# Performance work log

Hardware: AMD Instinct MI355X
Metric: run time of the kernel (lower is better)

Reference implementation:

```python
import jax, jax.numpy as jnp
import numpy as np
from jax import lax

B, S, E, H, V, C = 1024, 512, 128, 256, 128, 18


def setup_inputs() -> dict:
    key = jax.random.key(0)
    ks = jax.random.split(key, 12)
    x_in = jax.random.randint(ks[0], (B, S), 0, V, dtype=jnp.int32)
    x_lengths = jax.random.randint(ks[1], (B,), 1, S + 1, dtype=jnp.int32)
    emb = jax.random.normal(ks[2], (V, E), dtype=jnp.float32)
    emb = emb.at[0].set(0.0)  # padding_idx=0 row is zero
    k = 1.0 / np.sqrt(H)
    W_ih = jax.random.uniform(ks[3], (H, E), jnp.float32, -k, k)
    W_hh = jax.random.uniform(ks[4], (H, H), jnp.float32, -k, k)
    b_ih = jax.random.uniform(ks[5], (H,), jnp.float32, -k, k)
    b_hh = jax.random.uniform(ks[6], (H,), jnp.float32, -k, k)
    fc1_w = jax.random.uniform(ks[7], (H, H), jnp.float32, -k, k)
    fc1_b = jax.random.uniform(ks[8], (H,), jnp.float32, -k, k)
    kc = 1.0 / np.sqrt(H)
    fc2_w = jax.random.uniform(ks[9], (C, H), jnp.float32, -kc, kc)
    fc2_b = jax.random.uniform(ks[10], (C,), jnp.float32, -kc, kc)
    return dict(x_in=x_in, x_lengths=x_lengths, emb=emb, W_ih=W_ih, W_hh=W_hh,
                b_ih=b_ih, b_hh=b_hh, fc1_w=fc1_w, fc1_b=fc1_b,
                fc2_w=fc2_w, fc2_b=fc2_b)


def reference(x_in, x_lengths, emb, W_ih, W_hh, b_ih, b_hh, fc1_w, fc1_b, fc2_w, fc2_b):
    # Embedding lookup: [B,S] -> [B,S,E]
    x_emb = emb[x_in]
    # time-major for scan: [S,B,E]
    xt = jnp.transpose(x_emb, (1, 0, 2))

    def step(h, x_t):
        # Elman RNNCell: h' = tanh(x W_ih^T + b_ih + h W_hh^T + b_hh)
        h_new = jnp.tanh(x_t @ W_ih.T + b_ih + h @ W_hh.T + b_hh)
        return h_new, h_new

    h0 = jnp.zeros((x_in.shape[0], W_hh.shape[0]), dtype=x_emb.dtype)
    _, hiddens = lax.scan(step, h0, xt)  # [S,B,H]

    # column_gather: last valid hidden state per example
    idx = x_lengths.astype(jnp.int32) - 1
    y = hiddens[idx, jnp.arange(x_in.shape[0])]  # [B,H]

    # dropout omitted (deterministic / eval-mode reference)
    y = jax.nn.relu(y @ fc1_w.T + fc1_b)
    y = y @ fc2_w.T + fc2_b  # [B,C]; apply_activator=False
    return y
```

## Files before the change

kernel.cpp:

```cpp
#include <hip/hip_runtime.h>

#define Bb 1024
#define Ss 512
#define Ee 128
#define Hh 256
#define Vv 128
#define Cc 18

#define HB1  2048
#define YOFF 4096
#define ZOFF 8192

typedef __attribute__((ext_vector_type(8))) short short8;
typedef __attribute__((ext_vector_type(4))) float f32x4;
typedef __attribute__((ext_vector_type(2))) int int2v;

__device__ __forceinline__ unsigned short f2bf(float f) {
  union { float f; unsigned u; } v; v.f = f;
  return (unsigned short)((v.u + 0x7FFFu + ((v.u >> 16) & 1u)) >> 16);
}

__device__ __forceinline__ f32x4 mfma16(short8 a, short8 b, f32x4 c) {
  return __builtin_amdgcn_mfma_f32_16x16x32_bf16(a, b, c, 0, 0, 0);
}

__device__ __forceinline__ float ftanh(float x) {
  float e2 = __expf(2.0f * x);
  return 1.0f - 2.0f * __builtin_amdgcn_rcpf(e2 + 1.0f);
}

__device__ __forceinline__ unsigned cvtpk(float a, float b) {
  unsigned r;
  asm("v_cvt_pk_bf16_f32 %0, %1, %2" : "=v"(r) : "v"(a), "v"(b));
  return r;
}

__device__ __forceinline__ void load_wfrags2(const float* __restrict__ W, int j0, int l15, int g,
                                             short8 wfrag[2][8]) {
#pragma unroll
  for (int mt = 0; mt < 2; ++mt) {
    const float* wrow = W + (j0 + mt * 16 + l15) * Hh;
#pragma unroll
    for (int kt = 0; kt < 8; ++kt) {
      const float* wp = wrow + kt * 32 + g * 8;
      f32x4 a = *(const f32x4*)(wp);
      f32x4 b = *(const f32x4*)(wp + 4);
      short8 f;
      f[0] = (short)f2bf(a.x); f[1] = (short)f2bf(a.y);
      f[2] = (short)f2bf(a.z); f[3] = (short)f2bf(a.w);
      f[4] = (short)f2bf(b.x); f[5] = (short)f2bf(b.y);
      f[6] = (short)f2bf(b.z); f[7] = (short)f2bf(b.w);
      wfrag[mt][kt] = f;
    }
  }
}

__global__ void prep_T(const float* __restrict__ emb, const float* __restrict__ W_ih,
                       const float* __restrict__ b_ih, const float* __restrict__ b_hh,
                       float* __restrict__ T) {
  __shared__ float elds[Ee];
  const int v = blockIdx.x, j = threadIdx.x;
  if (j < Ee) elds[j] = emb[v * Ee + j];
  __syncthreads();
  float s = b_ih[j] + b_hh[j];
  const float* wr = W_ih + j * Ee;
#pragma unroll 8
  for (int e = 0; e < Ee; e += 4) {
    f32x4 w = *(const f32x4*)(wr + e);
    f32x4 x = *(const f32x4*)(elds + e);
    s += w.x * x.x + w.y * x.y + w.z * x.z + w.w * x.w;
  }
  T[v * Hh + j] = s;
}

template <int PAR>
__device__ __forceinline__ void step_phase(char* smem, const short8 (&wf)[2][8],
                                           const int (&roff)[8], const int (&woff)[2],
                                           const float* __restrict__ T,
                                           const int* __restrict__ xrow,
                                           int t, int mylen, int j0, int g, bool vr,
                                           f32x4 (&tcur)[2], int& xv_use, int& xv_inf) {
  char* RB = smem + (PAR ? HB1 : 0);
  char* WB = smem + (PAR ? 0 : HB1);

  const float* tp = T + xv_use * Hh + j0 + g * 4;
  f32x4 tn0 = *(const f32x4*)(tp);
  f32x4 tn1 = *(const f32x4*)(tp + 16);
  const int xv_new = xrow[min(t + 3, Ss - 1)];

  short8 hf[8];
  hf[0] = *(const short8*)(RB + roff[0]);
  hf[1] = *(const short8*)(RB + roff[1]);

  f32x4 aA[2], aB[2];
  const f32x4 Z4 = {0.f, 0.f, 0.f, 0.f};
  aA[0] = tcur[0]; aA[1] = tcur[1]; aB[0] = Z4; aB[1] = Z4;

#pragma unroll
  for (int kt = 0; kt < 8; ++kt) {
    if (kt < 6) hf[kt + 2] = *(const short8*)(RB + roff[kt + 2]);
    if ((kt & 1) == 0) {
      aA[0] = mfma16(wf[0][kt], hf[kt], aA[0]);
      aA[1] = mfma16(wf[1][kt], hf[kt], aA[1]);
    } else {
      aB[0] = mfma16(wf[0][kt], hf[kt], aB[0]);
      aB[1] = mfma16(wf[1][kt], hf[kt], aB[1]);
    }
  }

  const bool emit = (t == mylen - 1);
#pragma unroll
  for (int mt = 0; mt < 2; ++mt) {
    float s0 = aA[mt].x + aB[mt].x;
    float s1 = aA[mt].y + aB[mt].y;
    float s2 = aA[mt].z + aB[mt].z;
    float s3 = aA[mt].w + aB[mt].w;
    int2v pk;
    pk.x = (int)cvtpk(ftanh(s0), ftanh(s1));
    pk.y = (int)cvtpk(ftanh(s2), ftanh(s3));
    if (vr) {
      *(int2v*)(WB + woff[mt]) = pk;
      if (emit) *(int2v*)(smem + YOFF + woff[mt]) = pk;
    }
  }

  tcur[0] = tn0; tcur[1] = tn1;
  xv_use = xv_inf;
  xv_inf = xv_new;

  asm volatile("s_waitcnt lgkmcnt(0)" ::: "memory");
  __builtin_amdgcn_sched_barrier(0);
  __builtin_amdgcn_s_barrier();
  __builtin_amdgcn_sched_barrier(0);
}

__global__ __launch_bounds__(512, 2)
void rnn_fused(const int* __restrict__ x_in, const int* __restrict__ x_len,
               const float* __restrict__ W_hh, const float* __restrict__ T,
               const float* __restrict__ fc1_w, const float* __restrict__ fc1_b,
               const float* __restrict__ fc2_w, const float* __restrict__ fc2_b,
               float* __restrict__ out) {
  __shared__ __align__(16) char smem[12288];

  const int tid  = threadIdx.x;
  const int lane = tid & 63;
  const int wave = tid >> 6;
  const int l15  = lane & 15;
  const int g    = lane >> 4;
  const int j0   = wave * 32;
  const int grow = blockIdx.x * 4;
  const int r    = l15;
  const int rr   = r & 3;
  const bool vr  = (r < 4);

  short8 wfrag[2][8];
  load_wfrags2(W_hh, j0, l15, g, wfrag);

  const int mylen = x_len[grow + rr];
  int maxlen = 1;
#pragma unroll
  for (int i = 0; i < 4; ++i) maxlen = max(maxlen, x_len[grow + i]);

  ((int*)smem)[tid < 512 ? tid : 0] = 0;

  int roff[8], woff[2];
#pragma unroll
  for (int kt = 0; kt < 8; ++kt) roff[kt] = rr * 512 + ((kt * 64 + g * 16) ^ (rr << 6));
#pragma unroll
  for (int mt = 0; mt < 2; ++mt)
    woff[mt] = rr * 512 + (((j0 + mt * 16 + g * 4) * 2) ^ (rr << 6));

  const int* xrow = x_in + (grow + rr) * Ss;
  f32x4 tcur[2];
  {
    const int xv0 = xrow[0];
    const float* tp = T + xv0 * Hh + j0 + g * 4;
    tcur[0] = *(const f32x4*)(tp);
    tcur[1] = *(const f32x4*)(tp + 16);
  }
  int xv_use = xrow[min(1, Ss - 1)];
  int xv_inf = xrow[min(2, Ss - 1)];

  __syncthreads();

  const int mx2 = (maxlen + 1) & ~1;
  for (int t = 0; t < mx2; t += 2) {
    step_phase<0>(smem, wfrag, roff, woff, T, xrow, t,     mylen, j0, g, vr, tcur, xv_use, xv_inf);
    step_phase<1>(smem, wfrag, roff, woff, T, xrow, t + 1, mylen, j0, g, vr, tcur, xv_use, xv_inf);
  }

  short8 ffrag[2][8];
  load_wfrags2(fc1_w, j0, l15, g, ffrag);
  f32x4 fb[2];
#pragma unroll
  for (int mt = 0; mt < 2; ++mt)
    fb[mt] = *(const f32x4*)(fc1_b + j0 + mt * 16 + g * 4);

  short8 yf[8];
#pragma unroll
  for (int kt = 0; kt < 8; ++kt) yf[kt] = *(const short8*)(smem + YOFF + roff[kt]);

  const f32x4 Z4 = {0.f, 0.f, 0.f, 0.f};
  f32x4 acc[2], acc2[2];
#pragma unroll
  for (int mt = 0; mt < 2; ++mt) { acc[mt] = fb[mt]; acc2[mt] = Z4; }
#pragma unroll
  for (int kt = 0; kt < 4; ++kt)
#pragma unroll
    for (int mt = 0; mt < 2; ++mt)
      acc[mt] = mfma16(ffrag[mt][kt], yf[kt], acc[mt]);
#pragma unroll
  for (int kt = 4; kt < 8; ++kt)
#pragma unroll
    for (int mt = 0; mt < 2; ++mt)
      acc2[mt] = mfma16(ffrag[mt][kt], yf[kt], acc2[mt]);

  float* z_ld = (float*)(smem + ZOFF);
#pragma unroll
  for (int mt = 0; mt < 2; ++mt) {
    f32x4 z;
    z.x = fmaxf(acc[mt].x + acc2[mt].x, 0.f);
    z.y = fmaxf(acc[mt].y + acc2[mt].y, 0.f);
    z.z = fmaxf(acc[mt].z + acc2[mt].z, 0.f);
    z.w = fmaxf(acc[mt].w + acc2[mt].w, 0.f);
    if (vr) *(f32x4*)(z_ld + rr * 256 + j0 + mt * 16 + g * 4) = z;
  }
  __syncthreads();

  for (int idx = tid; idx < 4 * Cc; idx += 512) {
    const int r2 = idx / Cc, c = idx % Cc;
    float s = fc2_b[c];
    const float* wr2 = fc2_w + c * Hh;
    const float* zr  = z_ld + r2 * 256;
#pragma unroll 4
    for (int k = 0; k < Hh; k += 4) {
      f32x4 w = *(const f32x4*)(wr2 + k);
      f32x4 z = *(const f32x4*)(zr + k);
      s += w.x * z.x + w.y * z.y + w.z * z.z + w.w * z.w;
    }
    out[(grow + r2) * Cc + c] = s;
  }
}

extern "C" void kernel_launch(void* const* d_in, const int* in_sizes, int n_in,
                              void* d_out, int out_size, void* d_ws, size_t ws_size,
                              hipStream_t stream) {
  const int*   x_in  = (const int*)d_in[0];
  const int*   x_len = (const int*)d_in[1];
  const float* emb   = (const float*)d_in[2];
  const float* W_ih  = (const float*)d_in[3];
  const float* W_hh  = (const float*)d_in[4];
  const float* b_ih  = (const float*)d_in[5];
  const float* b_hh  = (const float*)d_in[6];
  const float* fc1_w = (const float*)d_in[7];
  const float* fc1_b = (const float*)d_in[8];
  const float* fc2_w = (const float*)d_in[9];
  const float* fc2_b = (const float*)d_in[10];
  float* out = (float*)d_out;

  float* T = (float*)d_ws;

  prep_T<<<Vv, Hh, 0, stream>>>(emb, W_ih, b_ih, b_hh, T);
  rnn_fused<<<Bb / 4, 512, 0, stream>>>(x_in, x_len, W_hh, T,
                                        fc1_w, fc1_b, fc2_w, fc2_b, out);
}
```

Before: 405.0 us.

## Split hidden dimension across 16 waves with one M-tile per wave

Doubles the block size from 512 to 1024 threads so each wave owns 16 hidden units instead of 32. Each wave now issues half as many MFMAs per timestep, which shortens the serial critical path of each recurrent step. The cost is more waves joining every per-step barrier, and the launch bounds now request higher occupancy, which caps register use. The T-row prefetch is reduced to one f32x4 and double-buffered through swapped references, and the shared-memory footprint shrinks.

```diff
diff --git a/kernel.cpp b/kernel.cpp
--- a/kernel.cpp
+++ b/kernel.cpp
@@ -9,7 +9,7 @@
 
 #define HB1  2048
 #define YOFF 4096
-#define ZOFF 8192
+#define ZOFF 6144
 
 typedef __attribute__((ext_vector_type(8))) short short8;
 typedef __attribute__((ext_vector_type(4))) float f32x4;
@@ -35,23 +35,20 @@
   return r;
 }
 
-__device__ __forceinline__ void load_wfrags2(const float* __restrict__ W, int j0, int l15, int g,
-                                             short8 wfrag[2][8]) {
-#pragma unroll
-  for (int mt = 0; mt < 2; ++mt) {
-    const float* wrow = W + (j0 + mt * 16 + l15) * Hh;
-#pragma unroll
-    for (int kt = 0; kt < 8; ++kt) {
-      const float* wp = wrow + kt * 32 + g * 8;
-      f32x4 a = *(const f32x4*)(wp);
-      f32x4 b = *(const f32x4*)(wp + 4);
-      short8 f;
-      f[0] = (short)f2bf(a.x); f[1] = (short)f2bf(a.y);
-      f[2] = (short)f2bf(a.z); f[3] = (short)f2bf(a.w);
-      f[4] = (short)f2bf(b.x); f[5] = (short)f2bf(b.y);
-      f[6] = (short)f2bf(b.z); f[7] = (short)f2bf(b.w);
-      wfrag[mt][kt] = f;
-    }
+__device__ __forceinline__ void load_wfrags1(const float* __restrict__ W, int j0, int l15, int g,
+                                             short8 (&wfrag)[8]) {
+  const float* wrow = W + (j0 + l15) * Hh;
+#pragma unroll
+  for (int kt = 0; kt < 8; ++kt) {
+    const float* wp = wrow + kt * 32 + g * 8;
+    f32x4 a = *(const f32x4*)(wp);
+    f32x4 b = *(const f32x4*)(wp + 4);
+    short8 f;
+    f[0] = (short)f2bf(a.x); f[1] = (short)f2bf(a.y);
+    f[2] = (short)f2bf(a.z); f[3] = (short)f2bf(a.w);
+    f[4] = (short)f2bf(b.x); f[5] = (short)f2bf(b.y);
+    f[6] = (short)f2bf(b.z); f[7] = (short)f2bf(b.w);
+    wfrag[kt] = f;
   }
 }
 
@@ -74,110 +71,91 @@
 }
 
 template <int PAR>
-__device__ __forceinline__ void step_phase(char* smem, const short8 (&wf)[2][8],
-                                           const int (&roff)[8], const int (&woff)[2],
+__device__ __forceinline__ void step_phase(char* smem, const short8 (&wf)[8],
+                                           const int (&roff)[8], int woff,
                                            const float* __restrict__ T,
                                            const int* __restrict__ xrow,
                                            int t, int mylen, int j0, int g, bool vr,
-                                           f32x4 (&tcur)[2], int& xv_use, int& xv_inf) {
+                                           f32x4& t_use, f32x4& t_load,
+                                           int& xv_use, int& xv_inf) {
   char* RB = smem + (PAR ? HB1 : 0);
   char* WB = smem + (PAR ? 0 : HB1);
 
-  const float* tp = T + xv_use * Hh + j0 + g * 4;
-  f32x4 tn0 = *(const f32x4*)(tp);
-  f32x4 tn1 = *(const f32x4*)(tp + 16);
+  t_load = *(const f32x4*)(T + xv_use * Hh + j0 + g * 4);
   const int xv_new = xrow[min(t + 3, Ss - 1)];
 
   short8 hf[8];
   hf[0] = *(const short8*)(RB + roff[0]);
   hf[1] = *(const short8*)(RB + roff[1]);
 
-  f32x4 aA[2], aB[2];
   const f32x4 Z4 = {0.f, 0.f, 0.f, 0.f};
-  aA[0] = tcur[0]; aA[1] = tcur[1]; aB[0] = Z4; aB[1] = Z4;
-
+  f32x4 aA, aB;
 #pragma unroll
   for (int kt = 0; kt < 8; ++kt) {
     if (kt < 6) hf[kt + 2] = *(const short8*)(RB + roff[kt + 2]);
-    if ((kt & 1) == 0) {
-      aA[0] = mfma16(wf[0][kt], hf[kt], aA[0]);
-      aA[1] = mfma16(wf[1][kt], hf[kt], aA[1]);
-    } else {
-      aB[0] = mfma16(wf[0][kt], hf[kt], aB[0]);
-      aB[1] = mfma16(wf[1][kt], hf[kt], aB[1]);
-    }
+    if (kt == 0)            aA = mfma16(wf[0], hf[0], t_use);
+    else if (kt == 1)       aB = mfma16(wf[1], hf[1], Z4);
+    else if ((kt & 1) == 0) aA = mfma16(wf[kt], hf[kt], aA);
+    else                    aB = mfma16(wf[kt], hf[kt], aB);
   }
 
   const bool emit = (t == mylen - 1);
-#pragma unroll
-  for (int mt = 0; mt < 2; ++mt) {
-    float s0 = aA[mt].x + aB[mt].x;
-    float s1 = aA[mt].y + aB[mt].y;
-    float s2 = aA[mt].z + aB[mt].z;
-    float s3 = aA[mt].w + aB[mt].w;
-    int2v pk;
-    pk.x = (int)cvtpk(ftanh(s0), ftanh(s1));
-    pk.y = (int)cvtpk(ftanh(s2), ftanh(s3));
-    if (vr) {
-      *(int2v*)(WB + woff[mt]) = pk;
-      if (emit) *(int2v*)(smem + YOFF + woff[mt]) = pk;
-    }
-  }
-
-  tcur[0] = tn0; tcur[1] = tn1;
+  float s0 = aA.x + aB.x;
+  float s1 = aA.y + aB.y;
+  float s2 = aA.z + aB.z;
+  float s3 = aA.w + aB.w;
+  int2v pk;
+  pk.x = (int)cvtpk(ftanh(s0), ftanh(s1));
+  pk.y = (int)cvtpk(ftanh(s2), ftanh(s3));
+  if (vr) {
+    *(int2v*)(WB + woff) = pk;
+    if (emit) *(int2v*)(smem + YOFF + woff) = pk;
+  }
+
   xv_use = xv_inf;
   xv_inf = xv_new;
 
   asm volatile("s_waitcnt lgkmcnt(0)" ::: "memory");
   __builtin_amdgcn_sched_barrier(0);
   __builtin_amdgcn_s_barrier();
-  __builtin_amdgcn_sched_barrier(0);
-}
-
-__global__ __launch_bounds__(512, 2)
+}
+
+__global__ __launch_bounds__(1024, 4)
 void rnn_fused(const int* __restrict__ x_in, const int* __restrict__ x_len,
                const float* __restrict__ W_hh, const float* __restrict__ T,
                const float* __restrict__ fc1_w, const float* __restrict__ fc1_b,
                const float* __restrict__ fc2_w, const float* __restrict__ fc2_b,
                float* __restrict__ out) {
-  __shared__ __align__(16) char smem[12288];
+  __shared__ __align__(16) char smem[10240];
 
   const int tid  = threadIdx.x;
   const int lane = tid & 63;
   const int wave = tid >> 6;
   const int l15  = lane & 15;
   const int g    = lane >> 4;
-  const int j0   = wave * 32;
+  const int j0   = wave * 16;
   const int grow = blockIdx.x * 4;
-  const int r    = l15;
-  const int rr   = r & 3;
-  const bool vr  = (r < 4);
-
-  short8 wfrag[2][8];
-  load_wfrags2(W_hh, j0, l15, g, wfrag);
+  const int rr   = l15 & 3;
+  const bool vr  = (l15 < 4);
+
+  short8 wfrag[8];
+  load_wfrags1(W_hh, j0, l15, g, wfrag);
 
   const int mylen = x_len[grow + rr];
   int maxlen = 1;
 #pragma unroll
   for (int i = 0; i < 4; ++i) maxlen = max(maxlen, x_len[grow + i]);
 
-  ((int*)smem)[tid < 512 ? tid : 0] = 0;
-
-  int roff[8], woff[2];
+  if (tid < 512) ((int*)smem)[tid] = 0;
+
+  int roff[8];
 #pragma unroll
   for (int kt = 0; kt < 8; ++kt) roff[kt] = rr * 512 + ((kt * 64 + g * 16) ^ (rr << 6));
-#pragma unroll
-  for (int mt = 0; mt < 2; ++mt)
-    woff[mt] = rr * 512 + (((j0 + mt * 16 + g * 4) * 2) ^ (rr << 6));
+  const int woff = rr * 512 + (((j0 + g * 4) * 2) ^ (rr << 6));
 
   const int* xrow = x_in + (grow + rr) * Ss;
-  f32x4 tcur[2];
-  {
-    const int xv0 = xrow[0];
-    const float* tp = T + xv0 * Hh + j0 + g * 4;
-    tcur[0] = *(const f32x4*)(tp);
-    tcur[1] = *(const f32x4*)(tp + 16);
-  }
+  f32x4 tA, tB;
+  tA = *(const f32x4*)(T + xrow[0] * Hh + j0 + g * 4);
   int xv_use = xrow[min(1, Ss - 1)];
   int xv_inf = xrow[min(2, Ss - 1)];
 
@@ -185,50 +163,41 @@
 
   const int mx2 = (maxlen + 1) & ~1;
   for (int t = 0; t < mx2; t += 2) {
-    step_phase<0>(smem, wfrag, roff, woff, T, xrow, t,     mylen, j0, g, vr, tcur, xv_use, xv_inf);
-    step_phase<1>(smem, wfrag, roff, woff, T, xrow, t + 1, mylen, j0, g, vr, tcur, xv_use, xv_inf);
-  }
-
-  short8 ffrag[2][8];
-  load_wfrags2(fc1_w, j0, l15, g, ffrag);
-  f32x4 fb[2];
-#pragma unroll
-  for (int mt = 0; mt < 2; ++mt)
-    fb[mt] = *(const f32x4*)(fc1_b + j0 + mt * 16 + g * 4);
+    step_phase<0>(smem, wfrag, roff, woff, T, xrow, t,     mylen, j0, g, vr, tA, tB, xv_use, xv_inf);
+    step_phase<1>(smem, wfrag, roff, woff, T, xrow, t + 1, mylen, j0, g, vr, tB, tA, xv_use, xv_inf);
+  }
+
+  short8 ffrag[8];
+  load_wfrags1(fc1_w, j0, l15, g, ffrag);
+  const f32x4 fb = *(const f32x4*)(fc1_b + j0 + g * 4);
 
   short8 yf[8];
 #pragma unroll
   for (int kt = 0; kt < 8; ++kt) yf[kt] = *(const short8*)(smem + YOFF + roff[kt]);
 
   const f32x4 Z4 = {0.f, 0.f, 0.f, 0.f};
-  f32x4 acc[2], acc2[2];
-#pragma unroll
-  for (int mt = 0; mt < 2; ++mt) { acc[mt] = fb[mt]; acc2[mt] = Z4; }
-#pragma unroll
-  for (int kt = 0; kt < 4; ++kt)
-#pragma unroll
-    for (int mt = 0; mt < 2; ++mt)
-      acc[mt] = mfma16(ffrag[mt][kt], yf[kt], acc[mt]);
-#pragma unroll
-  for (int kt = 4; kt < 8; ++kt)
-#pragma unroll
-    for (int mt = 0; mt < 2; ++mt)
-      acc2[mt] = mfma16(ffrag[mt][kt], yf[kt], acc2[mt]);
+  f32x4 aA, aB;
+#pragma unroll
+  for (int kt = 0; kt < 8; ++kt) {
+    if (kt == 0)            aA = mfma16(ffrag[0], yf[0], fb);
+    else if (kt == 1)       aB = mfma16(ffrag[1], yf[1], Z4);
+    else if ((kt & 1) == 0) aA = mfma16(ffrag[kt], yf[kt], aA);
+    else                    aB = mfma16(ffrag[kt], yf[kt], aB);
+  }
 
   float* z_ld = (float*)(smem + ZOFF);
-#pragma unroll
-  for (int mt = 0; mt < 2; ++mt) {
+  {
     f32x4 z;
-    z.x = fmaxf(acc[mt].x + acc2[mt].x, 0.f);
-    z.y = fmaxf(acc[mt].y + acc2[mt].y, 0.f);
-    z.z = fmaxf(acc[mt].z + acc2[mt].z, 0.f);
-    z.w = fmaxf(acc[mt].w + acc2[mt].w, 0.f);
-    if (vr) *(f32x4*)(z_ld + rr * 256 + j0 + mt * 16 + g * 4) = z;
+    z.x = fmaxf(aA.x + aB.x, 0.f);
+    z.y = fmaxf(aA.y + aB.y, 0.f);
+    z.z = fmaxf(aA.z + aB.z, 0.f);
+    z.w = fmaxf(aA.w + aB.w, 0.f);
+    if (vr) *(f32x4*)(z_ld + rr * 256 + j0 + g * 4) = z;
   }
   __syncthreads();
 
-  for (int idx = tid; idx < 4 * Cc; idx += 512) {
-    const int r2 = idx / Cc, c = idx % Cc;
+  if (tid < 4 * Cc) {
+    const int r2 = tid / Cc, c = tid % Cc;
     float s = fc2_b[c];
     const float* wr2 = fc2_w + c * Hh;
     const float* zr  = z_ld + r2 * 256;
@@ -261,6 +230,6 @@
   float* T = (float*)d_ws;
 
   prep_T<<<Vv, Hh, 0, stream>>>(emb, W_ih, b_ih, b_hh, T);
-  rnn_fused<<<Bb / 4, 512, 0, stream>>>(x_in, x_len, W_hh, T,
-                                        fc1_w, fc1_b, fc2_w, fc2_b, out);
-}
+  rnn_fused<<<Bb / 4, 1024, 0, stream>>>(x_in, x_len, W_hh, T,
+                                         fc1_w, fc1_b, fc2_w, fc2_b, out);
+}
```

Result: faster. 379.4 us (-6.3%).
